# Kernel tuning notes

Hardware: AMD Instinct MI355X
Metric: run time of the kernel (lower is better)

## Reference

```python
import jax, jax.numpy as jnp
import numpy as np

N = 4096; D0 = 1024; D1 = 1280; H0 = 819; H1 = 1024; S = 819; K = 5


def setup_inputs() -> dict:
    key = jax.random.key(0)
    ks = jax.random.split(key, 20)
    def rn(k, shape, scale=1.0):
        return jax.random.normal(k, shape, dtype=jnp.float32) * scale
    inp = {}
    inp['x0'] = rn(ks[0], (N, D0))
    inp['x1'] = rn(ks[1], (N, D1))
    inp['we'] = jax.random.uniform(ks[2], (N, 2), dtype=jnp.float32, minval=0.1, maxval=1.0)
    # scale graphs ~1/100 so row-aggregated features stay in tanh's linear-ish range
    inp['g0'] = rn(ks[3], (N, N), 0.01)
    inp['g1'] = rn(ks[4], (N, N), 0.01)
    # Linear weights stored [in, out] (torch Linear applies x @ W.T + b); xavier-ish scale
    inp['We1_0'] = rn(ks[5], (D0, H0), D0 ** -0.5); inp['be1_0'] = jnp.zeros((H0,), jnp.float32)
    inp['We2_0'] = rn(ks[6], (H0, S), H0 ** -0.5);  inp['be2_0'] = jnp.zeros((S,), jnp.float32)
    inp['We1_1'] = rn(ks[7], (D1, H1), D1 ** -0.5); inp['be1_1'] = jnp.zeros((H1,), jnp.float32)
    inp['We2_1'] = rn(ks[8], (H1, S), H1 ** -0.5);  inp['be2_1'] = jnp.zeros((S,), jnp.float32)
    inp['Wd1_0'] = rn(ks[9], (S, H0), S ** -0.5);   inp['bd1_0'] = jnp.zeros((H0,), jnp.float32)
    inp['Wd2_0'] = rn(ks[10], (H0, D0), H0 ** -0.5); inp['bd2_0'] = jnp.zeros((D0,), jnp.float32)
    inp['Wd1_1'] = rn(ks[11], (S, H1), S ** -0.5);  inp['bd1_1'] = jnp.zeros((H1,), jnp.float32)
    inp['Wd2_1'] = rn(ks[12], (H1, D1), H1 ** -0.5); inp['bd2_1'] = jnp.zeros((D1,), jnp.float32)
    inp['Ww_0'] = rn(ks[13], (S, S), S ** -0.5)
    inp['Ww_1'] = rn(ks[14], (S, S), S ** -0.5)
    inp['Wf_0'] = rn(ks[15], (S, S), S ** -0.5)
    inp['Wf_1'] = rn(ks[16], (S, S), S ** -0.5)
    # stands in for the sklearn spectral-clustering centers (constant w.r.t. autodiff)
    inp['cluster_layer'] = rn(ks[17], (K, S), 0.1)
    return inp


def _gconv2(g, x, W1, b1, W2, b2):
    # tanh(Linear(g @ x)) twice: fusable gather-MLP chain
    h1 = jnp.tanh((g @ x) @ W1 + b1)
    return jnp.tanh((g @ h1) @ W2 + b2)


def reference(x0, x1, we, g0, g1,
              We1_0, be1_0, We2_0, be2_0, We1_1, be1_1, We2_1, be2_1,
              Wd1_0, bd1_0, Wd2_0, bd2_0, Wd1_1, bd1_1, Wd2_1, bd2_1,
              Ww_0, Ww_1, Wf_0, Wf_1, cluster_layer):
    # encoders
    h2_0 = _gconv2(g0, x0, We1_0, be1_0, We2_0, be2_0)  # [N, S]
    h2_1 = _gconv2(g1, x1, We1_1, be1_1, We2_1, be2_1)  # [N, S]
    # diag(we[:,i]) @ h_i  ==  broadcast row-scale (avoids O(N^2) diag matmul)
    weighted_sum = we[:, 0:1] * h2_0 + we[:, 1:2] * h2_1
    z = weighted_sum / jnp.sum(we, axis=1, keepdims=True)  # diag(1/sum) @ ws
    # inner-product adjacency decoders
    adj0 = jax.nn.sigmoid((z @ Ww_0) @ z.T)  # [N, N]
    adj1 = jax.nn.sigmoid((z @ Ww_1) @ z.T)
    # feature decoders with fusion weights
    rec0 = _gconv2(g0, jnp.tanh(z @ Wf_0), Wd1_0, bd1_0, Wd2_0, bd2_0)  # [N, D0]
    rec1 = _gconv2(g1, jnp.tanh(z @ Wf_1), Wd1_1, bd1_1, Wd2_1, bd2_1)  # [N, D1]
    # Student-t soft assignment to cluster centers
    d2 = jnp.sum((z[:, None, :] - cluster_layer[None, :, :]) ** 2, axis=2)  # [N, K]
    q = 1.0 / (1.0 + d2)
    q = q / jnp.sum(q, axis=1, keepdims=True)
    # target distribution p
    w = q ** 2 / jnp.sum(q, axis=0)
    p = w / jnp.sum(w, axis=1, keepdims=True)
    return (rec0, rec1, adj0, adj1, z, p, q, cluster_layer)
```

## Files before the change

kernel.cpp:

```cpp
#include <hip/hip_runtime.h>
#include <hip/hip_bf16.h>
#include <cstdint>
#include <cstddef>

typedef __bf16 bf16;
typedef __attribute__((ext_vector_type(8))) __bf16 bf16x8;
typedef __attribute__((ext_vector_type(4))) __bf16 bf16x4;
typedef __attribute__((ext_vector_type(4))) float f32x4;

__device__ __forceinline__ void gload_lds16(const void* g, void* l) {
  __builtin_amdgcn_global_load_lds(
      (const __attribute__((address_space(1))) uint32_t*)(uintptr_t)g,
      (__attribute__((address_space(3))) uint32_t*)(uintptr_t)l, 16, 0, 0);
}

struct GProb {
  const bf16* A; const bf16* Bt; const float* bias;
  float* Cf; bf16* Cb; float* Cp;
  int K, Npad, ldcf, ldcb, Ntrue, act;
};
struct GBatch { GProb p[4]; };

template<int SPLIT>
__global__ __launch_bounds__(256, 2)
void gemm_nt_batch(GBatch b)
{
  const int prob = (SPLIT == 2) ? ((int)blockIdx.z >> 1) : (int)blockIdx.z;
  const int kz   = (SPLIT == 2) ? ((int)blockIdx.z & 1) : 0;
  const GProb P = b.p[prob];
  const long bn = (long)blockIdx.x * 128;
  if (bn >= P.Npad) return;

  __shared__ __align__(16) bf16 As[128 * 32];
  __shared__ __align__(16) bf16 Bs[128 * 32];

  const int K    = P.K;
  const int tid  = threadIdx.x;
  const int lane = tid & 63, wave = tid >> 6;
  const int wr = wave >> 1, wc = wave & 1;
  const int l15 = lane & 15, quad = lane >> 4;
  const long bm = (long)blockIdx.y * 128;

  long aoff[2], boff[2];
  int ldsoff[2];
#pragma unroll
  for (int s = 0; s < 2; ++s) {
    int slot = s * 256 + tid;
    int row = slot >> 2, cs = slot & 3;
    int gc = (cs ^ (row & 3) ^ ((row >> 2) & 3)) & 3;
    aoff[s] = (bm + row) * (long)K + gc * 8;
    boff[s] = (bn + row) * (long)K + gc * 8;
    ldsoff[s] = (s * 256 + wave * 64) * 8;
  }

  const int cfr = ((quad ^ (lane & 3) ^ ((lane >> 2) & 3)) & 3) * 8;
  int afr[4], bfr[4];
#pragma unroll
  for (int i = 0; i < 4; ++i) {
    afr[i] = (wr * 64 + i * 16 + l15) * 32 + cfr;
    bfr[i] = (wc * 64 + i * 16 + l15) * 32 + cfr;
  }

  f32x4 acc[4][4];
#pragma unroll
  for (int i = 0; i < 4; ++i)
#pragma unroll
    for (int j = 0; j < 4; ++j) acc[i][j] = {0.f, 0.f, 0.f, 0.f};

  const int Kseg = K / SPLIT;
  const int kbeg = kz * Kseg;
  for (int k0 = kbeg; k0 < kbeg + Kseg; k0 += 32) {
    __syncthreads();
    gload_lds16(P.A + aoff[0] + k0, As + ldsoff[0]);
    gload_lds16(P.A + aoff[1] + k0, As + ldsoff[1]);
    gload_lds16(P.Bt + boff[0] + k0, Bs + ldsoff[0]);
    gload_lds16(P.Bt + boff[1] + k0, Bs + ldsoff[1]);
    __syncthreads();

    bf16x8 av[4], bv[4];
#pragma unroll
    for (int i = 0; i < 4; ++i) av[i] = *(const bf16x8*)(As + afr[i]);
#pragma unroll
    for (int j = 0; j < 4; ++j) bv[j] = *(const bf16x8*)(Bs + bfr[j]);
#pragma unroll
    for (int i = 0; i < 4; ++i)
#pragma unroll
      for (int j = 0; j < 4; ++j)
        acc[i][j] = __builtin_amdgcn_mfma_f32_16x16x32_bf16(av[i], bv[j], acc[i][j], 0, 0, 0);
  }

  const long row0 = bm + wr * 64 + quad * 4;
  const long col0 = bn + wc * 64 + l15;
  if constexpr (SPLIT == 2) {
    float* Cp = P.Cp + (long)kz * 4096 * P.Npad;
#pragma unroll
    for (int i = 0; i < 4; ++i)
#pragma unroll
      for (int j = 0; j < 4; ++j)
#pragma unroll
        for (int t = 0; t < 4; ++t)
          Cp[(row0 + i * 16 + t) * (long)P.Npad + col0 + j * 16] = acc[i][j][t];
  } else {
    const int act = P.act;
#pragma unroll
    for (int i = 0; i < 4; ++i) {
#pragma unroll
      for (int j = 0; j < 4; ++j) {
        long c = col0 + j * 16;
        float bb = P.bias ? P.bias[c] : 0.f;
#pragma unroll
        for (int t = 0; t < 4; ++t) {
          long r = row0 + i * 16 + t;
          float v = acc[i][j][t] + bb;
          if (act == 1) v = tanhf(v);
          else if (act == 2) v = 1.f / (1.f + __expf(-v));
          if (P.Cf && c < P.Ntrue) P.Cf[r * P.ldcf + c] = v;
          if (P.Cb) P.Cb[r * P.ldcb + c] = (bf16)v;
        }
      }
    }
  }
}

struct CProb {
  const float* part; const float* bias;
  float* Cf; bf16* Cb;
  int Npad, ldcf, ldcb, Ntrue, act;
};
struct CBatch { CProb p[2]; };

__global__ void combine_batch(CBatch cb)
{
  const CProb P = cb.p[blockIdx.z];
  const int row = blockIdx.x;
  const int c4 = threadIdx.x * 4;
  if (c4 >= P.Npad) return;
  const long base = (long)row * P.Npad + c4;
  float4 a = *(const float4*)(P.part + base);
  float4 b = *(const float4*)(P.part + (long)4096 * P.Npad + base);
  float v[4] = {a.x + b.x, a.y + b.y, a.z + b.z, a.w + b.w};
  if (P.bias) {
    float4 bi = *(const float4*)(P.bias + c4);
    v[0] += bi.x; v[1] += bi.y; v[2] += bi.z; v[3] += bi.w;
  }
#pragma unroll
  for (int t = 0; t < 4; ++t) {
    if (P.act == 1) v[t] = tanhf(v[t]);
    else if (P.act == 2) v[t] = 1.f / (1.f + __expf(-v[t]));
  }
  if (P.Cf && c4 < P.Ntrue) {
    float* o = P.Cf + (long)row * P.ldcf + c4;
    o[0] = v[0]; o[1] = v[1]; o[2] = v[2]; o[3] = v[3];
  }
  if (P.Cb) {
    bf16x4 o = {(bf16)v[0], (bf16)v[1], (bf16)v[2], (bf16)v[3]};
    *(bf16x4*)(P.Cb + (long)row * P.ldcb + c4) = o;
  }
}

struct TrBatch {
  const void* src[14]; bf16* dst[14];
  int R[14], C[14], Q[14], nbx[14], isb[14];
  int blkStart[15];
  int nprob;
};

__global__ void tr_batch(TrBatch a)
{
  __shared__ float tile[32][33];
  int pi = 0, b = blockIdx.x;
  while (b >= a.blkStart[pi + 1]) ++pi;
  const int rel = b - a.blkStart[pi];
  const int nbx = a.nbx[pi];
  const int q0 = (rel % nbx) * 32;
  const int p0 = (rel / nbx) * 32;
  const int R = a.R[pi], C = a.C[pi], Q = a.Q[pi];
  const bool isb = a.isb[pi] != 0;
  const void* src = a.src[pi];
  const int tx = threadIdx.x & 31, ty = threadIdx.x >> 5;
#pragma unroll
  for (int y = ty; y < 32; y += 8) {
    int r = q0 + y, c = p0 + tx;
    float v = 0.f;
    if (r < R && c < C)
      v = isb ? (float)((const bf16*)src)[(long)r * C + c]
              : ((const float*)src)[(long)r * C + c];
    tile[y][tx] = v;
  }
  __syncthreads();
  bf16* dst = a.dst[pi];
#pragma unroll
  for (int y = ty; y < 32; y += 8)
    dst[(long)(p0 + y) * Q + (q0 + tx)] = (bf16)tile[tx][y];
}

struct CvtB { const float* s[4]; bf16* d[4]; long n[4]; };
__global__ void cvt_batch(CvtB cb)
{
  const float* s = cb.s[blockIdx.z];
  bf16* d = cb.d[blockIdx.z];
  long i = ((long)blockIdx.x * blockDim.x + threadIdx.x) * 4;
  if (i >= cb.n[blockIdx.z]) return;
  float4 v = *(const float4*)(s + i);
  bf16x4 o = {(bf16)v.x, (bf16)v.y, (bf16)v.z, (bf16)v.w};
  *(bf16x4*)(d + i) = o;
}

__global__ void zkern(const float* __restrict__ h20, const float* __restrict__ h21,
                      const float* __restrict__ we, float* __restrict__ zout,
                      bf16* __restrict__ zb)
{
  const int n = blockIdx.x;
  const float w0 = we[n * 2], w1 = we[n * 2 + 1];
  const float inv = 1.f / (w0 + w1);
  for (int c = threadIdx.x; c < 896; c += 256) {
    float v = (w0 * h20[(long)n * 896 + c] + w1 * h21[(long)n * 896 + c]) * inv;
    zb[(long)n * 896 + c] = (bf16)v;
    if (c < 819) zout[(long)n * 819 + c] = v;
  }
}

__global__ void qkern(const float* __restrict__ z, const float* __restrict__ cl,
                      float* __restrict__ qout)
{
  const int n = blockIdx.x;
  const int lane = threadIdx.x;
  float d0 = 0, d1 = 0, d2 = 0, d3 = 0, d4 = 0;
  for (int s = lane; s < 819; s += 64) {
    float zv = z[(long)n * 819 + s];
    float t0 = zv - cl[0 * 819 + s]; d0 += t0 * t0;
    float t1 = zv - cl[1 * 819 + s]; d1 += t1 * t1;
    float t2 = zv - cl[2 * 819 + s]; d2 += t2 * t2;
    float t3 = zv - cl[3 * 819 + s]; d3 += t3 * t3;
    float t4 = zv - cl[4 * 819 + s]; d4 += t4 * t4;
  }
#pragma unroll
  for (int off = 32; off > 0; off >>= 1) {
    d0 += __shfl_xor(d0, off);
    d1 += __shfl_xor(d1, off);
    d2 += __shfl_xor(d2, off);
    d3 += __shfl_xor(d3, off);
    d4 += __shfl_xor(d4, off);
  }
  if (lane == 0) {
    float q0 = 1.f / (1.f + d0), q1 = 1.f / (1.f + d1), q2 = 1.f / (1.f + d2);
    float q3 = 1.f / (1.f + d3), q4 = 1.f / (1.f + d4);
    float inv = 1.f / (q0 + q1 + q2 + q3 + q4);
    float* qr = qout + (long)n * 5;
    qr[0] = q0 * inv; qr[1] = q1 * inv; qr[2] = q2 * inv;
    qr[3] = q3 * inv; qr[4] = q4 * inv;
  }
}

__global__ void colsum_kern(const float* __restrict__ q, float* __restrict__ colsum)
{
  __shared__ float red[256];
  const int k = blockIdx.x;
  float s = 0.f;
  for (int n = threadIdx.x; n < 4096; n += 256) s += q[(long)n * 5 + k];
  red[threadIdx.x] = s;
  __syncthreads();
  for (int w = 128; w > 0; w >>= 1) {
    if (threadIdx.x < w) red[threadIdx.x] += red[threadIdx.x + w];
    __syncthreads();
  }
  if (threadIdx.x == 0) colsum[k] = red[0];
}

__global__ void pkern(const float* __restrict__ q, const float* __restrict__ colsum,
                      float* __restrict__ p)
{
  int n = blockIdx.x * blockDim.x + threadIdx.x;
  if (n >= 4096) return;
  float w[5], s = 0.f;
#pragma unroll
  for (int k = 0; k < 5; ++k) {
    float qv = q[(long)n * 5 + k];
    w[k] = qv * qv / colsum[k];
    s += w[k];
  }
  float inv = 1.f / s;
#pragma unroll
  for (int k = 0; k < 5; ++k) p[(long)n * 5 + k] = w[k] * inv;
}

struct BiasArgs {
  const float* src[8];
  float* dst[8];
  int n[8];
  int np[8];
};

__global__ void biaspad(BiasArgs a)
{
  int b = blockIdx.x;
  for (int i = threadIdx.x; i < a.np[b]; i += blockDim.x)
    a.dst[b][i] = (i < a.n[b]) ? a.src[b][i] : 0.f;
}

extern "C" void kernel_launch(void* const* d_in, const int* in_sizes, int n_in,
                              void* d_out, int out_size, void* d_ws, size_t ws_size,
                              hipStream_t stream)
{
  (void)in_sizes; (void)n_in; (void)out_size; (void)ws_size;
  const float* x0    = (const float*)d_in[0];
  const float* x1    = (const float*)d_in[1];
  const float* we    = (const float*)d_in[2];
  const float* g0    = (const float*)d_in[3];
  const float* g1    = (const float*)d_in[4];
  const float* We1_0 = (const float*)d_in[5];
  const float* be1_0 = (const float*)d_in[6];
  const float* We2_0 = (const float*)d_in[7];
  const float* be2_0 = (const float*)d_in[8];
  const float* We1_1 = (const float*)d_in[9];
  const float* be1_1 = (const float*)d_in[10];
  const float* We2_1 = (const float*)d_in[11];
  const float* be2_1 = (const float*)d_in[12];
  const float* Wd1_0 = (const float*)d_in[13];
  const float* bd1_0 = (const float*)d_in[14];
  const float* Wd2_0 = (const float*)d_in[15];
  const float* bd2_0 = (const float*)d_in[16];
  const float* Wd1_1 = (const float*)d_in[17];
  const float* bd1_1 = (const float*)d_in[18];
  const float* Wd2_1 = (const float*)d_in[19];
  const float* bd2_1 = (const float*)d_in[20];
  const float* Ww0   = (const float*)d_in[21];
  const float* Ww1   = (const float*)d_in[22];
  const float* Wf0   = (const float*)d_in[23];
  const float* Wf1   = (const float*)d_in[24];
  const float* clus  = (const float*)d_in[25];
  float* out = (float*)d_out;

  const size_t OFF_REC0 = 0;
  const size_t OFF_REC1 = 4194304;
  const size_t OFF_ADJ0 = 9437184;
  const size_t OFF_ADJ1 = 26214400;
  const size_t OFF_Z    = 42991616;
  const size_t OFF_P    = 46346240;
  const size_t OFF_Q    = 46366720;
  const size_t OFF_CL   = 46387200;

  char* ws = (char*)d_ws;
  size_t off = 0;
  auto alloc = [&](size_t bytes) -> void* {
    off = (off + 255) & ~(size_t)255;
    void* p = ws + off;
    off += bytes;
    return p;
  };
  const long N = 4096;
  bf16* g0b   = (bf16*)alloc((size_t)N * 4096 * 2);
  bf16* g1b   = (bf16*)alloc((size_t)N * 4096 * 2);
  bf16* x0b   = (bf16*)alloc((size_t)N * 1024 * 2);
  bf16* x1b   = (bf16*)alloc((size_t)N * 1280 * 2);
  bf16* BTe10 = (bf16*)alloc((size_t)896 * 1024 * 2);
  bf16* BTe20 = (bf16*)alloc((size_t)896 * 896 * 2);
  bf16* BTe11 = (bf16*)alloc((size_t)1024 * 1280 * 2);
  bf16* BTe21 = (bf16*)alloc((size_t)896 * 1024 * 2);
  bf16* BTd10 = (bf16*)alloc((size_t)896 * 896 * 2);
  bf16* BTd20 = (bf16*)alloc((size_t)1024 * 896 * 2);
  bf16* BTd11 = (bf16*)alloc((size_t)1024 * 896 * 2);
  bf16* BTd21 = (bf16*)alloc((size_t)1280 * 1024 * 2);
  bf16* BTw0  = (bf16*)alloc((size_t)896 * 896 * 2);
  bf16* BTw1  = (bf16*)alloc((size_t)896 * 896 * 2);
  bf16* BTf0  = (bf16*)alloc((size_t)896 * 896 * 2);
  bf16* BTf1  = (bf16*)alloc((size_t)896 * 896 * 2);
  float* pbe10 = (float*)alloc(896 * 4);
  float* pbe20 = (float*)alloc(896 * 4);
  float* pbe11 = (float*)alloc(1024 * 4);
  float* pbe21 = (float*)alloc(896 * 4);
  float* pbd10 = (float*)alloc(896 * 4);
  float* pbd20 = (float*)alloc(1024 * 4);
  float* pbd11 = (float*)alloc(1024 * 4);
  float* pbd21 = (float*)alloc(1280 * 4);
  float* h20f  = (float*)alloc((size_t)N * 896 * 4);
  float* h21f  = (float*)alloc((size_t)N * 896 * 4);
  bf16* zb     = (bf16*)alloc((size_t)N * 896 * 2);
  float* colsum = (float*)alloc(64);
  bf16* xT0 = (bf16*)alloc((size_t)1024 * 4096 * 2);
  bf16* xT1 = (bf16*)alloc((size_t)1280 * 4096 * 2);
  bf16* u0  = (bf16*)alloc((size_t)N * 1024 * 2);
  bf16* u1  = (bf16*)alloc((size_t)N * 1280 * 2);
  bf16* h0  = (bf16*)alloc((size_t)N * 896 * 2);
  bf16* h1b = (bf16*)alloc((size_t)N * 1024 * 2);
  bf16* y0  = (bf16*)alloc((size_t)N * 896 * 2);
  bf16* y1  = (bf16*)alloc((size_t)N * 896 * 2);
  bf16* t0b = (bf16*)alloc((size_t)N * 896 * 2);
  bf16* t1b = (bf16*)alloc((size_t)N * 896 * 2);
  float* partA = (float*)alloc((size_t)2 * N * 1024 * 4);
  float* partB = (float*)alloc((size_t)2 * N * 1024 * 4);

  {
    CvtB cb;
    cb.s[0] = g0; cb.d[0] = g0b; cb.n[0] = N * 4096;
    cb.s[1] = g1; cb.d[1] = g1b; cb.n[1] = N * 4096;
    cb.s[2] = x0; cb.d[2] = x0b; cb.n[2] = N * 1024;
    cb.s[3] = x1; cb.d[3] = x1b; cb.n[3] = N * 1280;
    cvt_batch<<<dim3(16384, 1, 4), 256, 0, stream>>>(cb);
  }

  {
    TrBatch tb{};
    tb.nprob = 0; tb.blkStart[0] = 0;
    auto addTr = [&](const void* s, bf16* d, int R, int C, int P, int Q, int isb) {
      int i = tb.nprob++;
      tb.src[i] = s; tb.dst[i] = d;
      tb.R[i] = R; tb.C[i] = C; tb.Q[i] = Q; tb.isb[i] = isb;
      tb.nbx[i] = Q / 32;
      tb.blkStart[i + 1] = tb.blkStart[i] + (Q / 32) * (P / 32);
    };
    addTr(We1_0, BTe10, 1024, 819, 896, 1024, 0);
    addTr(We2_0, BTe20, 819, 819, 896, 896, 0);
    addTr(We1_1, BTe11, 1280, 1024, 1024, 1280, 0);
    addTr(We2_1, BTe21, 1024, 819, 896, 1024, 0);
    addTr(Wd1_0, BTd10, 819, 819, 896, 896, 0);
    addTr(Wd2_0, BTd20, 819, 1024, 1024, 896, 0);
    addTr(Wd1_1, BTd11, 819, 1024, 1024, 896, 0);
    addTr(Wd2_1, BTd21, 1024, 1280, 1280, 1024, 0);
    addTr(Ww0, BTw0, 819, 819, 896, 896, 0);
    addTr(Ww1, BTw1, 819, 819, 896, 896, 0);
    addTr(Wf0, BTf0, 819, 819, 896, 896, 0);
    addTr(Wf1, BTf1, 819, 819, 896, 896, 0);
    tr_batch<<<tb.blkStart[tb.nprob], 256, 0, stream>>>(tb);
  }

  BiasArgs ba;
  {
    const float* bsrc[8] = {be1_0, be2_0, be1_1, be2_1, bd1_0, bd2_0, bd1_1, bd2_1};
    float* bdst[8] = {pbe10, pbe20, pbe11, pbe21, pbd10, pbd20, pbd11, pbd21};
    int bn_[8] = {819, 819, 1024, 819, 819, 1024, 1024, 1280};
    int bnp[8] = {896, 896, 1024, 896, 896, 1024, 1024, 1280};
    for (int i = 0; i < 8; ++i) { ba.src[i] = bsrc[i]; ba.dst[i] = bdst[i]; ba.n[i] = bn_[i]; ba.np[i] = bnp[i]; }
  }
  biaspad<<<8, 256, 0, stream>>>(ba);

  GBatch gb{};
  int np = 0, maxN = 0;
  auto beg = [&]() { np = 0; maxN = 0; gb = GBatch{}; };
  auto add = [&](const bf16* A, const bf16* Bt, const float* bias,
                 float* Cf, int ldcf, bf16* Cb, int ldcb,
                 int K, int Npad, int Ntrue, int act) {
    gb.p[np].A = A; gb.p[np].Bt = Bt; gb.p[np].bias = bias;
    gb.p[np].Cf = Cf; gb.p[np].Cb = Cb; gb.p[np].Cp = nullptr;
    gb.p[np].K = K; gb.p[np].Npad = Npad;
    gb.p[np].ldcf = ldcf; gb.p[np].ldcb = ldcb;
    gb.p[np].Ntrue = Ntrue; gb.p[np].act = act;
    ++np;
    if (Npad > maxN) maxN = Npad;
  };
  auto addS = [&](const bf16* A, const bf16* Bt, float* Cp, int K, int Npad) {
    gb.p[np].A = A; gb.p[np].Bt = Bt; gb.p[np].bias = nullptr;
    gb.p[np].Cf = nullptr; gb.p[np].Cb = nullptr; gb.p[np].Cp = Cp;
    gb.p[np].K = K; gb.p[np].Npad = Npad;
    gb.p[np].ldcf = 0; gb.p[np].ldcb = 0; gb.p[np].Ntrue = 0; gb.p[np].act = 0;
    ++np;
    if (Npad > maxN) maxN = Npad;
  };
  auto goN = [&]() { gemm_nt_batch<1><<<dim3(maxN / 128, 32, np), 256, 0, stream>>>(gb); };
  auto goS = [&]() { gemm_nt_batch<2><<<dim3(maxN / 128, 32, np * 2), 256, 0, stream>>>(gb); };
  auto comb = [&](const float* bias0, float* Cf0, int ldf0, int Nt0, bf16* Cb0, int ldb0, int Np0, int act0,
                  const float* bias1, float* Cf1, int ldf1, int Nt1, bf16* Cb1, int ldb1, int Np1, int act1) {
    CBatch cb;
    cb.p[0] = {partA, bias0, Cf0, Cb0, Np0, ldf0, ldb0, Nt0, act0};
    cb.p[1] = {partB, bias1, Cf1, Cb1, Np1, ldf1, ldb1, Nt1, act1};
    combine_batch<<<dim3(4096, 1, 2), 256, 0, stream>>>(cb);
  };
  auto trb2 = [&](const bf16* s0, int C0, const bf16* s1, int C1) {
    TrBatch tb{};
    tb.nprob = 2; tb.blkStart[0] = 0;
    tb.src[0] = s0; tb.dst[0] = xT0; tb.R[0] = 4096; tb.C[0] = C0; tb.Q[0] = 4096;
    tb.isb[0] = 1; tb.nbx[0] = 128; tb.blkStart[1] = 128 * (C0 / 32);
    tb.src[1] = s1; tb.dst[1] = xT1; tb.R[1] = 4096; tb.C[1] = C1; tb.Q[1] = 4096;
    tb.isb[1] = 1; tb.nbx[1] = 128; tb.blkStart[2] = tb.blkStart[1] + 128 * (C1 / 32);
    tr_batch<<<tb.blkStart[2], 256, 0, stream>>>(tb);
  };

  beg();
  add(x0b, BTe10, nullptr, nullptr, 0, u0, 896, 1024, 896, 896, 0);
  add(x1b, BTe11, nullptr, nullptr, 0, u1, 1024, 1280, 1024, 1024, 0);
  goN();
  trb2(u0, 896, u1, 1024);
  beg();
  addS(g0b, xT0, partA, 4096, 896);
  addS(g1b, xT1, partB, 4096, 1024);
  goS();
  comb(pbe10, nullptr, 0, 0, h0, 896, 896, 1,
       pbe11, nullptr, 0, 0, h1b, 1024, 1024, 1);
  beg();
  add(h0, BTe20, nullptr, nullptr, 0, u0, 896, 896, 896, 896, 0);
  add(h1b, BTe21, nullptr, nullptr, 0, u1, 896, 1024, 896, 896, 0);
  goN();
  trb2(u0, 896, u1, 896);
  beg();
  addS(g0b, xT0, partA, 4096, 896);
  addS(g1b, xT1, partB, 4096, 896);
  goS();
  comb(pbe20, h20f, 896, 896, nullptr, 0, 896, 1,
       pbe21, h21f, 896, 896, nullptr, 0, 896, 1);

  zkern<<<4096, 256, 0, stream>>>(h20f, h21f, we, out + OFF_Z, zb);

  beg();
  add(zb, BTw0, nullptr, nullptr, 0, y0, 896, 896, 896, 896, 0);
  add(zb, BTw1, nullptr, nullptr, 0, y1, 896, 896, 896, 896, 0);
  add(zb, BTf0, nullptr, nullptr, 0, t0b, 896, 896, 896, 896, 1);
  add(zb, BTf1, nullptr, nullptr, 0, t1b, 896, 896, 896, 896, 1);
  goN();
  beg();
  add(y0, zb, nullptr, out + OFF_ADJ0, 4096, nullptr, 0, 896, 4096, 4096, 2);
  add(y1, zb, nullptr, out + OFF_ADJ1, 4096, nullptr, 0, 896, 4096, 4096, 2);
  goN();

  trb2(t0b, 896, t1b, 896);
  beg();
  addS(g0b, xT0, partA, 4096, 896);
  addS(g1b, xT1, partB, 4096, 896);
  goS();
  comb(nullptr, nullptr, 0, 0, u0, 896, 896, 0,
       nullptr, nullptr, 0, 0, u1, 896, 896, 0);
  beg();
  add(u0, BTd10, pbd10, nullptr, 0, h0, 896, 896, 896, 896, 1);
  add(u1, BTd11, pbd11, nullptr, 0, h1b, 1024, 896, 1024, 1024, 1);
  goN();
  trb2(h0, 896, h1b, 1024);
  beg();
  addS(g0b, xT0, partA, 4096, 896);
  addS(g1b, xT1, partB, 4096, 1024);
  goS();
  comb(nullptr, nullptr, 0, 0, u0, 896, 896, 0,
       nullptr, nullptr, 0, 0, u1, 1024, 1024, 0);
  beg();
  add(u0, BTd20, pbd20, out + OFF_REC0, 1024, nullptr, 0, 896, 1024, 1024, 1);
  add(u1, BTd21, pbd21, out + OFF_REC1, 1280, nullptr, 0, 1024, 1280, 1280, 1);
  goN();

  qkern<<<4096, 64, 0, stream>>>(out + OFF_Z, clus, out + OFF_Q);
  colsum_kern<<<5, 256, 0, stream>>>(out + OFF_Q, colsum);
  pkern<<<16, 256, 0, stream>>>(out + OFF_Q, colsum, out + OFF_P);
  hipMemcpyAsync(out + OFF_CL, (const void*)clus, 4095 * sizeof(float),
                 hipMemcpyDeviceToDevice, stream);
}
```

Baseline: 1.272 ms.

## Remap GEMM blocks across XCDs and fuse split-K combine with z computation

The GEMM kernel now remaps the flat block id so that consecutive logical tiles land on the same XCD chiplet, aiming to improve L2 reuse of shared A/B panels on the multi-die GPU. Separately, the split-K combine for the second encoder layer is fused with the weighted z computation into one kernel, removing the intermediate fp32 h2 buffers and one launch. The remap adds integer division overhead per block and changes scheduling order.

```diff
diff --git a/kernel.cpp b/kernel.cpp
--- a/kernel.cpp
+++ b/kernel.cpp
@@ -12,6 +12,12 @@
   __builtin_amdgcn_global_load_lds(
       (const __attribute__((address_space(1))) uint32_t*)(uintptr_t)g,
       (__attribute__((address_space(3))) uint32_t*)(uintptr_t)l, 16, 0, 0);
+}
+
+__device__ __forceinline__ float actf(float v, int act) {
+  if (act == 1) return tanhf(v);
+  if (act == 2) return 1.f / (1.f + __expf(-v));
+  return v;
 }
 
 struct GProb {
@@ -25,10 +31,21 @@
 __global__ __launch_bounds__(256, 2)
 void gemm_nt_batch(GBatch b)
 {
-  const int prob = (SPLIT == 2) ? ((int)blockIdx.z >> 1) : (int)blockIdx.z;
-  const int kz   = (SPLIT == 2) ? ((int)blockIdx.z & 1) : 0;
+  const int nx = gridDim.x, ny = gridDim.y, nzz = gridDim.z;
+  const int total = nx * ny * nzz;
+  const int fid = (int)blockIdx.x + nx * ((int)blockIdx.y + ny * (int)blockIdx.z);
+  const int q = total >> 3, r = total & 7;
+  const int xcd = fid & 7, idx = fid >> 3;
+  const int wid = (xcd < r ? xcd * (q + 1) : r * (q + 1) + (xcd - r) * q) + idx;
+  const int wx = wid % nx;
+  const int rest = wid / nx;
+  const int wy = rest % ny;
+  const int wz = rest / ny;
+
+  const int prob = (SPLIT == 2) ? (wz >> 1) : wz;
+  const int kz   = (SPLIT == 2) ? (wz & 1) : 0;
   const GProb P = b.p[prob];
-  const long bn = (long)blockIdx.x * 128;
+  const long bn = (long)wx * 128;
   if (bn >= P.Npad) return;
 
   __shared__ __align__(16) bf16 As[128 * 32];
@@ -39,7 +56,7 @@
   const int lane = tid & 63, wave = tid >> 6;
   const int wr = wave >> 1, wc = wave & 1;
   const int l15 = lane & 15, quad = lane >> 4;
-  const long bm = (long)blockIdx.y * 128;
+  const long bm = (long)wy * 128;
 
   long aoff[2], boff[2];
   int ldsoff[2];
@@ -111,9 +128,7 @@
 #pragma unroll
         for (int t = 0; t < 4; ++t) {
           long r = row0 + i * 16 + t;
-          float v = acc[i][j][t] + bb;
-          if (act == 1) v = tanhf(v);
-          else if (act == 2) v = 1.f / (1.f + __expf(-v));
+          float v = actf(acc[i][j][t] + bb, act);
           if (P.Cf && c < P.Ntrue) P.Cf[r * P.ldcf + c] = v;
           if (P.Cb) P.Cb[r * P.ldcb + c] = (bf16)v;
         }
@@ -144,10 +159,7 @@
     v[0] += bi.x; v[1] += bi.y; v[2] += bi.z; v[3] += bi.w;
   }
 #pragma unroll
-  for (int t = 0; t < 4; ++t) {
-    if (P.act == 1) v[t] = tanhf(v[t]);
-    else if (P.act == 2) v[t] = 1.f / (1.f + __expf(-v[t]));
-  }
+  for (int t = 0; t < 4; ++t) v[t] = actf(v[t], P.act);
   if (P.Cf && c4 < P.Ntrue) {
     float* o = P.Cf + (long)row * P.ldcf + c4;
     o[0] = v[0]; o[1] = v[1]; o[2] = v[2]; o[3] = v[3];
@@ -156,6 +168,35 @@
     bf16x4 o = {(bf16)v[0], (bf16)v[1], (bf16)v[2], (bf16)v[3]};
     *(bf16x4*)(P.Cb + (long)row * P.ldcb + c4) = o;
   }
+}
+
+__global__ void combz(const float* __restrict__ pA, const float* __restrict__ pB,
+                      const float* __restrict__ bA, const float* __restrict__ bB,
+                      const float* __restrict__ we, float* __restrict__ zout,
+                      bf16* __restrict__ zb)
+{
+  const int n = blockIdx.x;
+  const int c = threadIdx.x * 4;
+  const long base = (long)n * 896 + c;
+  const long half = (long)4096 * 896;
+  float4 a0 = *(const float4*)(pA + base);
+  float4 a1 = *(const float4*)(pA + half + base);
+  float4 b0 = *(const float4*)(pB + base);
+  float4 b1 = *(const float4*)(pB + half + base);
+  float4 ba = *(const float4*)(bA + c);
+  float4 bb = *(const float4*)(bB + c);
+  const float w0 = we[n * 2], w1 = we[n * 2 + 1];
+  const float inv = 1.f / (w0 + w1);
+  float h0[4] = {a0.x + a1.x + ba.x, a0.y + a1.y + ba.y, a0.z + a1.z + ba.z, a0.w + a1.w + ba.w};
+  float h1[4] = {b0.x + b1.x + bb.x, b0.y + b1.y + bb.y, b0.z + b1.z + bb.z, b0.w + b1.w + bb.w};
+  bf16x4 o;
+#pragma unroll
+  for (int t = 0; t < 4; ++t) {
+    float v = (w0 * tanhf(h0[t]) + w1 * tanhf(h1[t])) * inv;
+    o[t] = (bf16)v;
+    if (c + t < 819) zout[(long)n * 819 + c + t] = v;
+  }
+  *(bf16x4*)(zb + base) = o;
 }
 
 struct TrBatch {
@@ -204,20 +245,6 @@
   float4 v = *(const float4*)(s + i);
   bf16x4 o = {(bf16)v.x, (bf16)v.y, (bf16)v.z, (bf16)v.w};
   *(bf16x4*)(d + i) = o;
-}
-
-__global__ void zkern(const float* __restrict__ h20, const float* __restrict__ h21,
-                      const float* __restrict__ we, float* __restrict__ zout,
-                      bf16* __restrict__ zb)
-{
-  const int n = blockIdx.x;
-  const float w0 = we[n * 2], w1 = we[n * 2 + 1];
-  const float inv = 1.f / (w0 + w1);
-  for (int c = threadIdx.x; c < 896; c += 256) {
-    float v = (w0 * h20[(long)n * 896 + c] + w1 * h21[(long)n * 896 + c]) * inv;
-    zb[(long)n * 896 + c] = (bf16)v;
-    if (c < 819) zout[(long)n * 819 + c] = v;
-  }
 }
 
 __global__ void qkern(const float* __restrict__ z, const float* __restrict__ cl,
@@ -373,8 +400,6 @@
   float* pbd20 = (float*)alloc(1024 * 4);
   float* pbd11 = (float*)alloc(1024 * 4);
   float* pbd21 = (float*)alloc(1280 * 4);
-  float* h20f  = (float*)alloc((size_t)N * 896 * 4);
-  float* h21f  = (float*)alloc((size_t)N * 896 * 4);
   bf16* zb     = (bf16*)alloc((size_t)N * 896 * 2);
   float* colsum = (float*)alloc(64);
   bf16* xT0 = (bf16*)alloc((size_t)1024 * 4096 * 2);
@@ -495,10 +520,7 @@
   addS(g0b, xT0, partA, 4096, 896);
   addS(g1b, xT1, partB, 4096, 896);
   goS();
-  comb(pbe20, h20f, 896, 896, nullptr, 0, 896, 1,
-       pbe21, h21f, 896, 896, nullptr, 0, 896, 1);
-
-  zkern<<<4096, 256, 0, stream>>>(h20f, h21f, we, out + OFF_Z, zb);
+  combz<<<4096, 224, 0, stream>>>(partA, partB, pbe20, pbe21, we, out + OFF_Z, zb);
 
   beg();
   add(zb, BTw0, nullptr, nullptr, 0, y0, 896, 896, 896, 896, 0);
```

Result: faster. 1.109 ms (-12.8%).
